# Kernel optimization log

Hardware: AMD Instinct MI355X
Metric: run time of the kernel (lower is better)

Reference implementation:

```python
import jax, jax.numpy as jnp
import numpy as np

B, S, H, L = 64, 512, 1024, 9  # batch, seq_len, hidden_size, num_labels


def setup_inputs() -> dict:
    key = jax.random.key(0)
    ks = jax.random.split(key, 8)
    hidden = jax.random.normal(ks[0], (B, S, H), dtype=jnp.float32)
    W = jax.random.normal(ks[1], (L, H), dtype=jnp.float32) * 0.02
    b = jnp.zeros((L,), dtype=jnp.float32)
    # pytorch-crf initializes transitions uniform in [-0.1, 0.1]
    start_transitions = jax.random.uniform(ks[2], (L,), jnp.float32, -0.1, 0.1)
    end_transitions = jax.random.uniform(ks[3], (L,), jnp.float32, -0.1, 0.1)
    transitions = jax.random.uniform(ks[4], (L, L), jnp.float32, -0.1, 0.1)
    labels = jax.random.randint(ks[5], (B, S), 0, L)
    # variable lengths; first timestep always valid (required by pytorch-crf)
    lengths = jax.random.randint(ks[6], (B,), S // 4, S + 1)
    mask = (jnp.arange(S)[None, :] < lengths[:, None]).astype(jnp.int32)
    return {
        "hidden": hidden, "W": W, "b": b,
        "start_transitions": start_transitions,
        "end_transitions": end_transitions,
        "transitions": transitions,
        "labels": labels, "mask": mask,
    }


def reference(hidden, W, b, start_transitions, end_transitions, transitions, labels, mask):
    # classifier: emissions [B,S,L] (fp32, matching .float() cast in the module)
    emissions = jnp.einsum("bsh,lh->bsl", hidden, W) + b
    maskf = mask.astype(emissions.dtype)

    # ---- numerator: score of the gold path ----
    emit = jnp.take_along_axis(emissions, labels[..., None], axis=-1)[..., 0]  # [B,S]
    trans_sc = transitions[labels[:, :-1], labels[:, 1:]]                       # [B,S-1]
    score = (start_transitions[labels[:, 0]]
             + jnp.sum(emit * maskf, axis=1)
             + jnp.sum(trans_sc * maskf[:, 1:], axis=1))
    seq_ends = jnp.sum(mask, axis=1) - 1                     # last valid index per example
    last_tags = labels[jnp.arange(labels.shape[0]), seq_ends]
    score = score + end_transitions[last_tags]

    # ---- denominator: log partition via masked forward recurrence ----
    alpha0 = start_transitions[None, :] + emissions[:, 0]    # [B,L]
    em_t = jnp.swapaxes(emissions, 0, 1)[1:]                 # [S-1,B,L]
    mk_t = jnp.swapaxes(mask, 0, 1)[1:].astype(bool)         # [S-1,B]

    def step(alpha, xs):
        e_t, m_t = xs
        # broadcast: alpha[b,i] + transitions[i,j] + e_t[b,j]
        nxt = jax.scipy.special.logsumexp(
            alpha[:, :, None] + transitions[None, :, :] + e_t[:, None, :], axis=1)
        alpha = jnp.where(m_t[:, None], nxt, alpha)
        return alpha, None

    alpha, _ = jax.lax.scan(step, alpha0, (em_t, mk_t))
    logZ = jax.scipy.special.logsumexp(alpha + end_transitions[None, :], axis=1)  # [B]

    llh = score - logZ
    loss = -jnp.mean(llh)  # reduction='mean', negated in the module
    return loss
```

## Files before the change

kernel.cpp:

```cpp
#include <hip/hip_runtime.h>
#include <hip/hip_bf16.h>

#define LOG2E 1.4426950408889634f
#define LN2   0.6931471805599453f

constexpr int Bn = 64, Sn = 512, Hn = 1024, Ln = 9;
constexpr int CL = 24;
constexpr int NC = 22;

__device__ __forceinline__ float fexp2(float x) {
    float r; asm("v_exp_f32 %0, %1" : "=v"(r) : "v"(x)); return r;
}
__device__ __forceinline__ float flog2(float x) {
    float r; asm("v_log_f32 %0, %1" : "=v"(r) : "v"(x)); return r;
}
__device__ __forceinline__ float max9(const float* s) {
    return fmaxf(fmaxf(fmaxf(s[0], s[1]), fmaxf(s[2], s[3])),
                 fmaxf(fmaxf(s[4], s[5]), fmaxf(s[6], fmaxf(s[7], s[8]))));
}

__global__ __launch_bounds__(256) void emis_kernel(
    const float* __restrict__ hidden, const float* __restrict__ W,
    const float* __restrict__ bias, float* __restrict__ emis,
    float* __restrict__ out0)
{
    __shared__ float red[4][64][37];
    const int lane = threadIdx.x & 63;
    const int w    = threadIdx.x >> 6;
    const int r0   = (blockIdx.x * 4 + w) * 4;

    if (blockIdx.x == 0 && threadIdx.x == 0) out0[0] = 0.f;

    float acc[4][Ln];
    #pragma unroll
    for (int r = 0; r < 4; ++r)
        #pragma unroll
        for (int l = 0; l < Ln; ++l) acc[r][l] = 0.f;

    #pragma unroll 1
    for (int p = 0; p < 4; ++p) {
        const int h0 = p * 256 + lane * 4;
        float4 wv[Ln];
        #pragma unroll
        for (int l = 0; l < Ln; ++l)
            wv[l] = *(const float4*)(W + l * Hn + h0);
        #pragma unroll
        for (int r = 0; r < 4; ++r) {
            float4 h = *(const float4*)(hidden + (size_t)(r0 + r) * Hn + h0);
            #pragma unroll
            for (int l = 0; l < Ln; ++l) {
                acc[r][l] = fmaf(h.x, wv[l].x, acc[r][l]);
                acc[r][l] = fmaf(h.y, wv[l].y, acc[r][l]);
                acc[r][l] = fmaf(h.z, wv[l].z, acc[r][l]);
                acc[r][l] = fmaf(h.w, wv[l].w, acc[r][l]);
            }
        }
    }

    #pragma unroll
    for (int r = 0; r < 4; ++r)
        #pragma unroll
        for (int l = 0; l < Ln; ++l)
            red[w][lane][r * Ln + l] = acc[r][l];
    __syncthreads();

    if (lane < 36) {
        float s0 = 0.f, s1 = 0.f, s2 = 0.f, s3 = 0.f;
        #pragma unroll 4
        for (int i = 0; i < 64; i += 4) {
            s0 += red[w][i + 0][lane];
            s1 += red[w][i + 1][lane];
            s2 += red[w][i + 2][lane];
            s3 += red[w][i + 3][lane];
        }
        const int r = lane / 9, l = lane - r * 9;
        emis[(size_t)(r0 + r) * Ln + l] = (s0 + s1) + (s2 + s3) + bias[l];
    }
}

__global__ __launch_bounds__(256) void crf_kernel(
    const float* __restrict__ emis, const float* __restrict__ st,
    const float* __restrict__ et,   const float* __restrict__ T,
    const int* __restrict__ labels, const int* __restrict__ mask,
    float* __restrict__ out)
{
    __shared__ __align__(16) float e_lds[Sn * Ln];
    __shared__ float M_lds[NC][Ln][10];
    __shared__ float part[4];
    __shared__ int   sl_sh;

    const int b    = blockIdx.x;
    const int tid  = threadIdx.x;
    const int w    = tid >> 6;
    const int lane = tid & 63;

    {
        const float4* src = (const float4*)(emis + (size_t)b * Sn * Ln);
        float4* dst = (float4*)e_lds;
        for (int i = tid; i < (Sn * Ln) / 4; i += 256) dst[i] = src[i];
    }
    float E[Ln][Ln];
    #pragma unroll
    for (int k = 0; k < Ln; ++k)
        #pragma unroll
        for (int j = 0; j < Ln; ++j)
            E[k][j] = fexp2(T[k * Ln + j] * LOG2E);
    if (w == 3) {
        const int* mb = mask + b * Sn;
        int s = 0;
        #pragma unroll
        for (int r = 0; r < Sn / 64; ++r) s += mb[lane + r * 64];
        #pragma unroll
        for (int off = 32; off; off >>= 1) s += __shfl_xor(s, off);
        if (lane == 0) sl_sh = s;
    }
    __syncthreads();

    const int sl    = sl_sh;
    const int nreal = (sl - 1 + CL - 1) / CL;

    {
        const int ul = lane / 9;
        const int i  = lane - ul * 9;
        const int c  = w * 7 + ul;
        const int t0 = 1 + c * CL;
        if (ul < 7 && c < nreal) {
            const int nst = min(CL, sl - t0);
            float u[Ln];
            {
                const float* e0 = e_lds + t0 * Ln;
                #pragma unroll
                for (int j = 0; j < Ln; ++j)
                    u[j] = E[i][j] * fexp2(fmaf(e0[j], LOG2E, -4.f));
            }
            float extra = 0.f;
            for (int s = 1; s < nst; ++s) {
                const float* es = e_lds + (t0 + s) * Ln;
                float qn[Ln];
                #pragma unroll
                for (int j = 0; j < Ln; ++j)
                    qn[j] = fexp2(fmaf(es[j], LOG2E, -4.f));
                float v[Ln];
                #pragma unroll
                for (int j = 0; j < Ln; ++j) {
                    float a = u[0] * E[0][j];
                    #pragma unroll
                    for (int k = 1; k < Ln; ++k) a = fmaf(u[k], E[k][j], a);
                    v[j] = a;
                }
                #pragma unroll
                for (int j = 0; j < Ln; ++j) u[j] = v[j] * qn[j];
                if (s == 12) {
                    float m  = max9(u);
                    float iv = 1.f / m;
                    #pragma unroll
                    for (int j = 0; j < Ln; ++j) u[j] *= iv;
                    extra = flog2(m);
                }
            }
            #pragma unroll
            for (int j = 0; j < Ln; ++j)
                M_lds[c][i][j] = flog2(u[j]) + extra + 4.f * (float)nst;
        }
    }
    __syncthreads();

    float logZ = 0.f;
    if (w == 0) {
        const int j9 = lane < Ln ? lane : Ln - 1;
        float al[Ln];
        #pragma unroll
        for (int j = 0; j < Ln; ++j) al[j] = (st[j] + e_lds[j]) * LOG2E;
        for (int c = 0; c < nreal; ++c) {
            float s[Ln];
            #pragma unroll
            for (int k = 0; k < Ln; ++k) s[k] = al[k] + M_lds[c][k][j9];
            float p = max9(s);
            float sum = fexp2(s[0] - p);
            #pragma unroll
            for (int k = 1; k < Ln; ++k) sum += fexp2(s[k] - p);
            float aj = p + flog2(sum);
            #pragma unroll
            for (int k = 0; k < Ln; ++k) al[k] = __shfl(aj, k);
        }
        float z[Ln];
        #pragma unroll
        for (int j = 0; j < Ln; ++j) z[j] = al[j] + et[j] * LOG2E;
        float p = max9(z);
        float sum = fexp2(z[0] - p);
        #pragma unroll
        for (int j = 1; j < Ln; ++j) sum += fexp2(z[j] - p);
        logZ = (p + flog2(sum)) * LN2;
    } else {
        const int* lb = labels + b * Sn;
        float sc = 0.f;
        for (int t = (w - 1) * 64 + lane; t < sl; t += 192) {
            int lt = lb[t];
            sc += e_lds[t * Ln + lt];
            if (t >= 1) sc += T[lb[t - 1] * Ln + lt];
        }
        #pragma unroll
        for (int off = 32; off; off >>= 1) sc += __shfl_xor(sc, off);
        if (w == 1 && lane == 0) sc += st[lb[0]] + et[lb[sl - 1]];
        if (lane == 0) part[w - 1] = sc;
    }
    __syncthreads();

    if (w == 0 && lane == 0) {
        float llh = part[0] + part[1] + part[2] - logZ;
        atomicAdd(out, llh * (-1.f / 64.f));
    }
}

extern "C" void kernel_launch(void* const* d_in, const int* in_sizes, int n_in,
                              void* d_out, int out_size, void* d_ws, size_t ws_size,
                              hipStream_t stream) {
    const float* hidden = (const float*)d_in[0];
    const float* W      = (const float*)d_in[1];
    const float* bias   = (const float*)d_in[2];
    const float* st     = (const float*)d_in[3];
    const float* et     = (const float*)d_in[4];
    const float* T      = (const float*)d_in[5];
    const int*   labels = (const int*)d_in[6];
    const int*   mask   = (const int*)d_in[7];

    float* emis = (float*)d_ws;
    float* outp = (float*)d_out;

    emis_kernel<<<2048, 256, 0, stream>>>(hidden, W, bias, emis, outp);
    crf_kernel<<<Bn, 256, 0, stream>>>(emis, st, et, T, labels, mask, outp);
}
```

Measured before the change: 51.36 us.

## Fuse chunked CRF transfer-matrix products into the emission GEMM kernel

```diff
diff --git a/kernel.cpp b/kernel.cpp
--- a/kernel.cpp
+++ b/kernel.cpp
@@ -5,8 +5,8 @@
 #define LN2   0.6931471805599453f
 
 constexpr int Bn = 64, Sn = 512, Hn = 1024, Ln = 9;
-constexpr int CL = 24;
-constexpr int NC = 22;
+constexpr int RB = 16;
+constexpr int NK = 32;
 
 __device__ __forceinline__ float fexp2(float x) {
     float r; asm("v_exp_f32 %0, %1" : "=v"(r) : "v"(x)); return r;
@@ -19,17 +19,23 @@
                  fmaxf(fmaxf(s[4], s[5]), fmaxf(s[6], fmaxf(s[7], s[8]))));
 }
 
-__global__ __launch_bounds__(256) void emis_kernel(
+__global__ __launch_bounds__(256, 4) void emis_chunk_kernel(
     const float* __restrict__ hidden, const float* __restrict__ W,
-    const float* __restrict__ bias, float* __restrict__ emis,
-    float* __restrict__ out0)
+    const float* __restrict__ bias,   const float* __restrict__ T,
+    const int* __restrict__ labels,   const int* __restrict__ mask,
+    float* __restrict__ Mbuf, float* __restrict__ eL,
+    float* __restrict__ e0g,  float* __restrict__ out)
 {
     __shared__ float red[4][64][37];
-    const int lane = threadIdx.x & 63;
-    const int w    = threadIdx.x >> 6;
-    const int r0   = (blockIdx.x * 4 + w) * 4;
-
-    if (blockIdx.x == 0 && threadIdx.x == 0) out0[0] = 0.f;
+    __shared__ __align__(16) float e_s[RB][12];
+    __shared__ __align__(16) float E_lds[Ln][12];
+    __shared__ int sl_sh;
+
+    const int tid = threadIdx.x, w = tid >> 6, lane = tid & 63;
+    const int bid = blockIdx.x, b = bid >> 5, k = bid & 31;
+    const int r0  = b * Sn + k * RB;
+
+    if (bid == 0 && tid == 0) out[0] = 0.f;
 
     float acc[4][Ln];
     #pragma unroll
@@ -46,7 +52,7 @@
             wv[l] = *(const float4*)(W + l * Hn + h0);
         #pragma unroll
         for (int r = 0; r < 4; ++r) {
-            float4 h = *(const float4*)(hidden + (size_t)(r0 + r) * Hn + h0);
+            float4 h = *(const float4*)(hidden + (size_t)(r0 + w * 4 + r) * Hn + h0);
             #pragma unroll
             for (int l = 0; l < Ln; ++l) {
                 acc[r][l] = fmaf(h.x, wv[l].x, acc[r][l]);
@@ -55,6 +61,12 @@
                 acc[r][l] = fmaf(h.w, wv[l].w, acc[r][l]);
             }
         }
+    }
+
+    if (w == 1 && lane < Ln) {
+        #pragma unroll
+        for (int j = 0; j < Ln; ++j)
+            E_lds[lane][j] = fexp2(T[lane * Ln + j] * LOG2E);
     }
 
     #pragma unroll
@@ -73,39 +85,15 @@
             s2 += red[w][i + 2][lane];
             s3 += red[w][i + 3][lane];
         }
-        const int r = lane / 9, l = lane - r * 9;
-        emis[(size_t)(r0 + r) * Ln + l] = (s0 + s1) + (s2 + s3) + bias[l];
-    }
-}
-
-__global__ __launch_bounds__(256) void crf_kernel(
-    const float* __restrict__ emis, const float* __restrict__ st,
-    const float* __restrict__ et,   const float* __restrict__ T,
-    const int* __restrict__ labels, const int* __restrict__ mask,
-    float* __restrict__ out)
-{
-    __shared__ __align__(16) float e_lds[Sn * Ln];
-    __shared__ float M_lds[NC][Ln][10];
-    __shared__ float part[4];
-    __shared__ int   sl_sh;
-
-    const int b    = blockIdx.x;
-    const int tid  = threadIdx.x;
-    const int w    = tid >> 6;
-    const int lane = tid & 63;
-
-    {
-        const float4* src = (const float4*)(emis + (size_t)b * Sn * Ln);
-        float4* dst = (float4*)e_lds;
-        for (int i = tid; i < (Sn * Ln) / 4; i += 256) dst[i] = src[i];
-    }
-    float E[Ln][Ln];
-    #pragma unroll
-    for (int k = 0; k < Ln; ++k)
-        #pragma unroll
-        for (int j = 0; j < Ln; ++j)
-            E[k][j] = fexp2(T[k * Ln + j] * LOG2E);
-    if (w == 3) {
+        const int rr = lane / 9, l = lane - rr * 9;
+        const int tloc = w * 4 + rr;
+        const float v = (s0 + s1) + (s2 + s3) + bias[l];
+        e_s[tloc][l] = v;
+        const int t = k * RB + tloc;
+        if (l == labels[b * Sn + t]) eL[b * Sn + t] = v;
+        if (k == 0 && tloc == 0) e0g[b * Ln + l] = v;
+    }
+    if (w == 2) {
         const int* mb = mask + b * Sn;
         int s = 0;
         #pragma unroll
@@ -116,41 +104,65 @@
     }
     __syncthreads();
 
-    const int sl    = sl_sh;
-    const int nreal = (sl - 1 + CL - 1) / CL;
-
-    {
-        const int ul = lane / 9;
-        const int i  = lane - ul * 9;
-        const int c  = w * 7 + ul;
-        const int t0 = 1 + c * CL;
-        if (ul < 7 && c < nreal) {
-            const int nst = min(CL, sl - t0);
+    if (w == 0 && lane < Ln) {
+        const int sl  = sl_sh;
+        const int tb  = (k == 0) ? 1 : 0;
+        const int lim = min(RB, sl - k * RB);
+        const int nst = lim - tb;
+        if (nst > 0) {
+            const int i = lane;
+            float4 q0 = *(float4*)&e_s[tb][0];
+            float4 q1 = *(float4*)&e_s[tb][4];
+            float  q8 = e_s[tb][8];
+            float qn[Ln] = {
+                fexp2(fmaf(q0.x, LOG2E, -4.f)), fexp2(fmaf(q0.y, LOG2E, -4.f)),
+                fexp2(fmaf(q0.z, LOG2E, -4.f)), fexp2(fmaf(q0.w, LOG2E, -4.f)),
+                fexp2(fmaf(q1.x, LOG2E, -4.f)), fexp2(fmaf(q1.y, LOG2E, -4.f)),
+                fexp2(fmaf(q1.z, LOG2E, -4.f)), fexp2(fmaf(q1.w, LOG2E, -4.f)),
+                fexp2(fmaf(q8,   LOG2E, -4.f)) };
             float u[Ln];
             {
-                const float* e0 = e_lds + t0 * Ln;
-                #pragma unroll
-                for (int j = 0; j < Ln; ++j)
-                    u[j] = E[i][j] * fexp2(fmaf(e0[j], LOG2E, -4.f));
+                float4 a0 = *(float4*)&E_lds[i][0];
+                float4 a1 = *(float4*)&E_lds[i][4];
+                float  a8 = E_lds[i][8];
+                u[0] = a0.x * qn[0]; u[1] = a0.y * qn[1];
+                u[2] = a0.z * qn[2]; u[3] = a0.w * qn[3];
+                u[4] = a1.x * qn[4]; u[5] = a1.y * qn[5];
+                u[6] = a1.z * qn[6]; u[7] = a1.w * qn[7];
+                u[8] = a8   * qn[8];
             }
             float extra = 0.f;
             for (int s = 1; s < nst; ++s) {
-                const float* es = e_lds + (t0 + s) * Ln;
-                float qn[Ln];
-                #pragma unroll
-                for (int j = 0; j < Ln; ++j)
-                    qn[j] = fexp2(fmaf(es[j], LOG2E, -4.f));
+                q0 = *(float4*)&e_s[tb + s][0];
+                q1 = *(float4*)&e_s[tb + s][4];
+                q8 = e_s[tb + s][8];
+                qn[0] = fexp2(fmaf(q0.x, LOG2E, -4.f));
+                qn[1] = fexp2(fmaf(q0.y, LOG2E, -4.f));
+                qn[2] = fexp2(fmaf(q0.z, LOG2E, -4.f));
+                qn[3] = fexp2(fmaf(q0.w, LOG2E, -4.f));
+                qn[4] = fexp2(fmaf(q1.x, LOG2E, -4.f));
+                qn[5] = fexp2(fmaf(q1.y, LOG2E, -4.f));
+                qn[6] = fexp2(fmaf(q1.z, LOG2E, -4.f));
+                qn[7] = fexp2(fmaf(q1.w, LOG2E, -4.f));
+                qn[8] = fexp2(fmaf(q8,   LOG2E, -4.f));
                 float v[Ln];
                 #pragma unroll
-                for (int j = 0; j < Ln; ++j) {
-                    float a = u[0] * E[0][j];
-                    #pragma unroll
-                    for (int k = 1; k < Ln; ++k) a = fmaf(u[k], E[k][j], a);
-                    v[j] = a;
+                for (int j = 0; j < Ln; ++j) v[j] = 0.f;
+                #pragma unroll
+                for (int kk = 0; kk < Ln; ++kk) {
+                    float4 e0v = *(float4*)&E_lds[kk][0];
+                    float4 e1v = *(float4*)&E_lds[kk][4];
+                    float  e8  = E_lds[kk][8];
+                    const float uk = u[kk];
+                    v[0] = fmaf(uk, e0v.x, v[0]); v[1] = fmaf(uk, e0v.y, v[1]);
+                    v[2] = fmaf(uk, e0v.z, v[2]); v[3] = fmaf(uk, e0v.w, v[3]);
+                    v[4] = fmaf(uk, e1v.x, v[4]); v[5] = fmaf(uk, e1v.y, v[5]);
+                    v[6] = fmaf(uk, e1v.z, v[6]); v[7] = fmaf(uk, e1v.w, v[7]);
+                    v[8] = fmaf(uk, e8,   v[8]);
                 }
                 #pragma unroll
                 for (int j = 0; j < Ln; ++j) u[j] = v[j] * qn[j];
-                if (s == 12) {
+                if (s == 8) {
                     float m  = max9(u);
                     float iv = 1.f / m;
                     #pragma unroll
@@ -158,30 +170,62 @@
                     extra = flog2(m);
                 }
             }
+            float* o = Mbuf + (size_t)bid * 81 + i * Ln;
             #pragma unroll
             for (int j = 0; j < Ln; ++j)
-                M_lds[c][i][j] = flog2(u[j]) + extra + 4.f * (float)nst;
-        }
-    }
-    __syncthreads();
+                o[j] = flog2(u[j]) + extra + 4.f * (float)nst;
+        }
+    }
+}
+
+__global__ __launch_bounds__(256) void combine_kernel(
+    const float* __restrict__ st, const float* __restrict__ et,
+    const float* __restrict__ T,  const int* __restrict__ labels,
+    const int* __restrict__ mask, const float* __restrict__ Mbuf,
+    const float* __restrict__ eL, const float* __restrict__ e0g,
+    float* __restrict__ out)
+{
+    __shared__ float part[4];
+    const int b = blockIdx.x, tid = threadIdx.x;
+    const int w = tid >> 6, lane = tid & 63;
+
+    const int* mb = mask + b * Sn;
+    int sl = 0;
+    #pragma unroll
+    for (int r = 0; r < Sn / 64; ++r) sl += mb[lane + r * 64];
+    #pragma unroll
+    for (int off = 32; off; off >>= 1) sl += __shfl_xor(sl, off);
 
     float logZ = 0.f;
     if (w == 0) {
         const int j9 = lane < Ln ? lane : Ln - 1;
         float al[Ln];
         #pragma unroll
-        for (int j = 0; j < Ln; ++j) al[j] = (st[j] + e_lds[j]) * LOG2E;
-        for (int c = 0; c < nreal; ++c) {
+        for (int j = 0; j < Ln; ++j) al[j] = (st[j] + e0g[b * Ln + j]) * LOG2E;
+        const float* mcb = Mbuf + (size_t)(b * NK) * 81;
+        const int klast = (sl - 1) >> 4;
+        float col[Ln];
+        #pragma unroll
+        for (int i = 0; i < Ln; ++i) col[i] = mcb[i * Ln + j9];
+        for (int k = 0; k <= klast; ++k) {
+            float nc[Ln];
+            if (k < klast) {
+                const float* m2 = mcb + (size_t)(k + 1) * 81;
+                #pragma unroll
+                for (int i = 0; i < Ln; ++i) nc[i] = m2[i * Ln + j9];
+            }
             float s[Ln];
             #pragma unroll
-            for (int k = 0; k < Ln; ++k) s[k] = al[k] + M_lds[c][k][j9];
+            for (int i = 0; i < Ln; ++i) s[i] = al[i] + col[i];
             float p = max9(s);
             float sum = fexp2(s[0] - p);
             #pragma unroll
-            for (int k = 1; k < Ln; ++k) sum += fexp2(s[k] - p);
+            for (int i = 1; i < Ln; ++i) sum += fexp2(s[i] - p);
             float aj = p + flog2(sum);
             #pragma unroll
-            for (int k = 0; k < Ln; ++k) al[k] = __shfl(aj, k);
+            for (int i = 0; i < Ln; ++i) al[i] = __shfl(aj, i);
+            #pragma unroll
+            for (int i = 0; i < Ln; ++i) col[i] = nc[i];
         }
         float z[Ln];
         #pragma unroll
@@ -195,9 +239,8 @@
         const int* lb = labels + b * Sn;
         float sc = 0.f;
         for (int t = (w - 1) * 64 + lane; t < sl; t += 192) {
-            int lt = lb[t];
-            sc += e_lds[t * Ln + lt];
-            if (t >= 1) sc += T[lb[t - 1] * Ln + lt];
+            sc += eL[b * Sn + t];
+            if (t >= 1) sc += T[lb[t - 1] * Ln + lb[t]];
         }
         #pragma unroll
         for (int off = 32; off; off >>= 1) sc += __shfl_xor(sc, off);
@@ -206,7 +249,7 @@
     }
     __syncthreads();
 
-    if (w == 0 && lane == 0) {
+    if (tid == 0) {
         float llh = part[0] + part[1] + part[2] - logZ;
         atomicAdd(out, llh * (-1.f / 64.f));
     }
@@ -224,9 +267,12 @@
     const int*   labels = (const int*)d_in[6];
     const int*   mask   = (const int*)d_in[7];
 
-    float* emis = (float*)d_ws;
+    float* Mbuf = (float*)d_ws;
+    float* eLp  = Mbuf + (size_t)Bn * NK * 81;
+    float* e0g  = eLp + (size_t)Bn * Sn;
     float* outp = (float*)d_out;
 
-    emis_kernel<<<2048, 256, 0, stream>>>(hidden, W, bias, emis, outp);
-    crf_kernel<<<Bn, 256, 0, stream>>>(emis, st, et, T, labels, mask, outp);
-}
+    emis_chunk_kernel<<<Bn * NK, 256, 0, stream>>>(hidden, W, bias, T, labels, mask,
+                                                   Mbuf, eLp, e0g, outp);
+    combine_kernel<<<Bn, 256, 0, stream>>>(st, et, T, labels, mask, Mbuf, eLp, e0g, outp);
+}
```

Result: slower. 60.99 us (+18.7%).

## Compute emissions with bf16 MFMA and restructure CRF chunk inner loop

Applied to the files above, without the earlier changes.

```diff
diff --git a/kernel.cpp b/kernel.cpp
--- a/kernel.cpp
+++ b/kernel.cpp
@@ -8,11 +8,17 @@
 constexpr int CL = 24;
 constexpr int NC = 22;
 
+typedef __attribute__((ext_vector_type(8))) short short8v;
+typedef __attribute__((ext_vector_type(4))) float f32x4;
+
 __device__ __forceinline__ float fexp2(float x) {
     float r; asm("v_exp_f32 %0, %1" : "=v"(r) : "v"(x)); return r;
 }
 __device__ __forceinline__ float flog2(float x) {
     float r; asm("v_log_f32 %0, %1" : "=v"(r) : "v"(x)); return r;
+}
+__device__ __forceinline__ unsigned cvtpk(float lo, float hi) {
+    unsigned r; asm("v_cvt_pk_bf16_f32 %0, %1, %2" : "=v"(r) : "v"(lo), "v"(hi)); return r;
 }
 __device__ __forceinline__ float max9(const float* s) {
     return fmaxf(fmaxf(fmaxf(s[0], s[1]), fmaxf(s[2], s[3])),
@@ -24,61 +30,53 @@
     const float* __restrict__ bias, float* __restrict__ emis,
     float* __restrict__ out0)
 {
-    __shared__ float red[4][64][37];
-    const int lane = threadIdx.x & 63;
-    const int w    = threadIdx.x >> 6;
-    const int r0   = (blockIdx.x * 4 + w) * 4;
-
-    if (blockIdx.x == 0 && threadIdx.x == 0) out0[0] = 0.f;
-
-    float acc[4][Ln];
-    #pragma unroll
-    for (int r = 0; r < 4; ++r)
-        #pragma unroll
-        for (int l = 0; l < Ln; ++l) acc[r][l] = 0.f;
-
-    #pragma unroll 1
-    for (int p = 0; p < 4; ++p) {
-        const int h0 = p * 256 + lane * 4;
-        float4 wv[Ln];
-        #pragma unroll
-        for (int l = 0; l < Ln; ++l)
-            wv[l] = *(const float4*)(W + l * Hn + h0);
+    __shared__ __align__(16) unsigned short wfrag[32][64][8];
+    const int tid = threadIdx.x, lane = tid & 63, w = tid >> 6;
+
+    if (blockIdx.x == 0 && tid == 0) out0[0] = 0.f;
+
+    for (int f = tid; f < 32 * 64; f += 256) {
+        const int s = f >> 6, l = f & 63;
+        const int j = l & 15, k0 = s * 32 + ((l >> 4) << 3);
+        uint4 pk = {0u, 0u, 0u, 0u};
+        if (j < Ln) {
+            float4 a = *(const float4*)(W + j * Hn + k0);
+            float4 b = *(const float4*)(W + j * Hn + k0 + 4);
+            pk.x = cvtpk(a.x, a.y); pk.y = cvtpk(a.z, a.w);
+            pk.z = cvtpk(b.x, b.y); pk.w = cvtpk(b.z, b.w);
+        }
+        *(uint4*)&wfrag[s][l][0] = pk;
+    }
+    __syncthreads();
+
+    const int row0 = blockIdx.x * 64 + w * 16;
+    const float* hptr = hidden + (size_t)(row0 + (lane & 15)) * Hn + ((lane >> 4) << 3);
+
+    f32x4 acc = {0.f, 0.f, 0.f, 0.f};
+    #pragma unroll 4
+    for (int s = 0; s < 32; ++s) {
+        float4 a0 = *(const float4*)(hptr + s * 32);
+        float4 a1 = *(const float4*)(hptr + s * 32 + 4);
+        uint4 ap;
+        ap.x = cvtpk(a0.x, a0.y); ap.y = cvtpk(a0.z, a0.w);
+        ap.z = cvtpk(a1.x, a1.y); ap.w = cvtpk(a1.z, a1.w);
+        short8v A  = *(short8v*)&ap;
+        short8v Bv = *(const short8v*)&wfrag[s][lane][0];
+        acc = __builtin_amdgcn_mfma_f32_16x16x32_bf16(A, Bv, acc, 0, 0, 0);
+    }
+
+    const int col = lane & 15;
+    if (col < Ln) {
+        const float bv = bias[col];
         #pragma unroll
         for (int r = 0; r < 4; ++r) {
-            float4 h = *(const float4*)(hidden + (size_t)(r0 + r) * Hn + h0);
-            #pragma unroll
-            for (int l = 0; l < Ln; ++l) {
-                acc[r][l] = fmaf(h.x, wv[l].x, acc[r][l]);
-                acc[r][l] = fmaf(h.y, wv[l].y, acc[r][l]);
-                acc[r][l] = fmaf(h.z, wv[l].z, acc[r][l]);
-                acc[r][l] = fmaf(h.w, wv[l].w, acc[r][l]);
-            }
-        }
-    }
-
-    #pragma unroll
-    for (int r = 0; r < 4; ++r)
-        #pragma unroll
-        for (int l = 0; l < Ln; ++l)
-            red[w][lane][r * Ln + l] = acc[r][l];
-    __syncthreads();
-
-    if (lane < 36) {
-        float s0 = 0.f, s1 = 0.f, s2 = 0.f, s3 = 0.f;
-        #pragma unroll 4
-        for (int i = 0; i < 64; i += 4) {
-            s0 += red[w][i + 0][lane];
-            s1 += red[w][i + 1][lane];
-            s2 += red[w][i + 2][lane];
-            s3 += red[w][i + 3][lane];
-        }
-        const int r = lane / 9, l = lane - r * 9;
-        emis[(size_t)(r0 + r) * Ln + l] = (s0 + s1) + (s2 + s3) + bias[l];
-    }
-}
-
-__global__ __launch_bounds__(256) void crf_kernel(
+            const int row = ((lane >> 4) << 2) + r;
+            emis[(size_t)(row0 + row) * Ln + col] = acc[r] + bv;
+        }
+    }
+}
+
+__global__ __launch_bounds__(256, 1) void crf_kernel(
     const float* __restrict__ emis, const float* __restrict__ st,
     const float* __restrict__ et,   const float* __restrict__ T,
     const int* __restrict__ labels, const int* __restrict__ mask,
@@ -136,20 +134,22 @@
             float extra = 0.f;
             for (int s = 1; s < nst; ++s) {
                 const float* es = e_lds + (t0 + s) * Ln;
-                float qn[Ln];
+                float e2[Ln];
+                #pragma unroll
+                for (int j = 0; j < Ln; ++j) e2[j] = es[j];
+                float v[Ln];
+                #pragma unroll
+                for (int j = 0; j < Ln; ++j) v[j] = 0.f;
+                #pragma unroll
+                for (int kk = 0; kk < Ln; ++kk) {
+                    const float uk = u[kk];
+                    #pragma unroll
+                    for (int j = 0; j < Ln; ++j)
+                        v[j] = fmaf(uk, E[kk][j], v[j]);
+                }
                 #pragma unroll
                 for (int j = 0; j < Ln; ++j)
-                    qn[j] = fexp2(fmaf(es[j], LOG2E, -4.f));
-                float v[Ln];
-                #pragma unroll
-                for (int j = 0; j < Ln; ++j) {
-                    float a = u[0] * E[0][j];
-                    #pragma unroll
-                    for (int k = 1; k < Ln; ++k) a = fmaf(u[k], E[k][j], a);
-                    v[j] = a;
-                }
-                #pragma unroll
-                for (int j = 0; j < Ln; ++j) u[j] = v[j] * qn[j];
+                    u[j] = v[j] * fexp2(fmaf(e2[j], LOG2E, -4.f));
                 if (s == 12) {
                     float m  = max9(u);
                     float iv = 1.f / m;
@@ -227,6 +227,6 @@
     float* emis = (float*)d_ws;
     float* outp = (float*)d_out;
 
-    emis_kernel<<<2048, 256, 0, stream>>>(hidden, W, bias, emis, outp);
+    emis_kernel<<<512, 256, 0, stream>>>(hidden, W, bias, emis, outp);
     crf_kernel<<<Bn, 256, 0, stream>>>(emis, st, et, T, labels, mask, outp);
 }
```

Result: faster. 43.76 us (-14.8%).
